# Kernel optimization log

Measured on AMD Instinct MI355X. Metric: run time of the kernel, lower is better.

The kernel has to match this reference:

```python
import jax, jax.numpy as jnp
import numpy as np

# --- model dimensions ---
MAX_UP = 512; MAX_DOWN = 512; MAX_ELEC = MAX_UP + MAX_DOWN  # 1024 orbitals
N_NUC = 128
MAX_CHARGE = 16
TOT_ORB = MAX_CHARGE * (MAX_CHARGE + 1) // 2  # 136
NUM_HEADS = 8; D_HEAD = 32; F = NUM_HEADS * D_HEAD  # 256
L = 4          # num_layers
FN = 256       # nuc_feats dim
SIGMOID_SHIFTS = (2.0, 4.0, 6.0)
E_DIM = 3 + 1 + len(SIGMOID_SHIFTS)  # featurized edge dim = 7


def generate_spd_orbitals(charges):
    """Vectorized form of the scan/fori_loop scatter in the source.
    For nucleus n with charge c: orbitals[cum_charge+i, n, c(c-1)/2+i] = 1 for i<c.
    charges: [N_NUC] int. Returns [MAX_ELEC, N_NUC, TOT_ORB] float32."""
    c = charges.astype(jnp.int32)
    off = jnp.cumsum(c) - c                      # exclusive cumsum (cum_charge)
    prec = c * (c - 1) // 2                      # preceding orbital offset
    i = jnp.arange(MAX_CHARGE, dtype=jnp.int32)
    valid = (i[None, :] < c[:, None])            # [N_NUC, MAX_CHARGE]
    elec = jnp.clip(off[:, None] + i[None, :], 0, MAX_ELEC - 1)
    orbi = jnp.clip(prec[:, None] + i[None, :], 0, TOT_ORB - 1)
    nuc = jnp.broadcast_to(jnp.arange(N_NUC, dtype=jnp.int32)[:, None], (N_NUC, MAX_CHARGE))
    orb = jnp.zeros((MAX_ELEC, N_NUC, TOT_ORB), jnp.float32)
    return orb.at[elec.ravel(), nuc.ravel(), orbi.ravel()].add(valid.ravel().astype(jnp.float32))


def make_permutation(n_up, n_down):
    segments = [0, n_up, MAX_UP, MAX_UP + n_down, MAX_ELEC]
    updates = [0, n_down, -MAX_UP + n_up, 0]
    idx = jnp.arange(MAX_ELEC)
    agg = jnp.zeros_like(idx)
    for lft, r, u in zip(segments[:-1], segments[1:], updates):
        agg = agg + ((idx >= lft) & (idx < r)) * (idx + u)
    return agg


def featurize_real_space_vector(diffs):
    """[N,N,3] -> [N,N,7]: rescaled diffs, log1p(|r|), sigmoid(|r|-shift)."""
    norm = jnp.sqrt(jnp.sum(diffs * diffs, -1, keepdims=True) + 1e-12)
    sig = jnp.concatenate([jax.nn.sigmoid(norm - s) for s in SIGMOID_SHIFTS], -1)
    return jnp.concatenate([diffs / (1.0 + norm), jnp.log1p(norm), sig], -1)


def orb_ln(x):
    """OrbLayerNorm(feat_axis=-1, nuc_axis=1, eps=1.0) on [O, N, F] tensors."""
    mean = jnp.mean(x, -1, keepdims=True)
    var = jnp.var(x, -1, keepdims=True)
    max_var = jnp.max(var, axis=1, keepdims=True)
    return jax.lax.rsqrt(max_var + 1.0) * (x - mean)


def setup_inputs() -> dict:
    key = jax.random.key(0)
    ks = jax.random.split(key, 8)
    coords = jax.random.normal(ks[0], (N_NUC, 3), jnp.float32) * 3.0
    charges = jax.random.randint(ks[1], (N_NUC,), 0, 8)  # sum < MAX_ELEC
    nuc_mask = jnp.ones((N_NUC,), bool)
    nuc_feats = jax.random.normal(ks[2], (N_NUC, FN), jnp.float32)
    orb_mask = jnp.ones((MAX_ELEC,), bool)
    # hk.Linear(num_feats, with_bias=False, TruncatedNormal(stddev=1))
    W_orb = jax.random.truncated_normal(ks[3], -2.0, 2.0, (TOT_ORB, F), jnp.float32)
    W_edge = jax.random.normal(ks[4], (L, E_DIM, NUM_HEADS), jnp.float32) / np.sqrt(E_DIM)
    W_val = jax.random.normal(ks[5], (L, F, F), jnp.float32) / np.sqrt(F)
    W_nuc = jax.random.normal(ks[6], (L, FN, F), jnp.float32) / np.sqrt(FN)
    W_out = jax.random.normal(ks[7], (L, F, F), jnp.float32) / np.sqrt(F)
    return dict(coords=coords, charges=charges, nuc_mask=nuc_mask, n_up=500,
                n_down=480, nuc_feats=nuc_feats, orb_mask=orb_mask, W_orb=W_orb,
                W_edge=W_edge, W_val=W_val, W_nuc=W_nuc, W_out=W_out)


def reference(coords, charges, nuc_mask, n_up, n_down, nuc_feats, orb_mask,
              W_orb, W_edge, W_val, W_nuc, W_out):
    orbital_feats = generate_spd_orbitals(charges)               # [O, N, TOT_ORB]
    perm = make_permutation(int(n_up), int(n_down))
    orbital_feats = orbital_feats[perm]
    feats = jnp.einsum('ont,tf->onf', orbital_feats, W_orb)     # [O, N, F]
    m = (orb_mask[:, None, None] & nuc_mask[None, :, None]).astype(feats.dtype)
    feats = feats * m
    diffs = coords[:, None, :] - coords[None, :, :]              # [N, N, 3]
    nn_mask = nuc_mask[:, None] & nuc_mask[None, :]
    edge = featurize_real_space_vector(diffs) * nn_mask[..., None]  # [N, N, E]
    for l in range(L):
        # --- MaskedMPNNBlock ---
        h = orb_ln(feats)
        vals = jnp.einsum('onf,fg->ong', h, W_val[l]).reshape(MAX_ELEC, N_NUC, NUM_HEADS, D_HEAD)
        ew = jnp.einsum('ije,eh->ijh', edge, W_edge[l]) * nn_mask[..., None]
        msg = jnp.einsum('ijh,ojhd->oihd', ew, vals).reshape(MAX_ELEC, N_NUC, F)
        msg = msg + nuc_feats @ W_nuc[l]
        feats = feats + jnp.einsum('onf,fg->ong', jnp.tanh(orb_ln(msg)), W_out[l])
        feats = feats * m
    return feats
```

## Files before the change

kernel.cpp:

```cpp
#include <hip/hip_runtime.h>
#include <hip/hip_bf16.h>


#define O_TOT 1024

typedef __bf16 bf16x8 __attribute__((ext_vector_type(8)));
typedef float f32x4 __attribute__((ext_vector_type(4)));

static __device__ __forceinline__ unsigned short f2bf(float f) {
  __bf16 b = (__bf16)f;
  unsigned short u;
  __builtin_memcpy(&u, &b, 2);
  return u;
}
static __device__ __forceinline__ float ftanh(float x) {
  float e = __expf(2.f * x);
  return 1.f - 2.f * __builtin_amdgcn_rcpf(e + 1.f);
}

struct alignas(8) US4 { unsigned short a, b, c, d; };

static __device__ __forceinline__ int swzA(int row, int cb) {
  return row * 512 + (cb ^ ((row & 7) << 4) ^ (((row >> 3) & 1) << 5));
}
static __device__ __forceinline__ int swzV(int row, int cb) {
  return row * 256 + (cb ^ ((row & 7) << 4) ^ (((row >> 3) & 1) << 5));
}


__global__ void k_orbmap(const int* __restrict__ charges, const int* __restrict__ n_up_p,
                         const int* __restrict__ n_down_p, int* __restrict__ orb_nuc,
                         int* __restrict__ orb_t) {
  __shared__ int off[129];
  __shared__ int prec[128];
  int tid = threadIdx.x;
  if (tid == 0) {
    int a = 0;
    for (int n = 0; n < 128; ++n) { off[n] = a; a += charges[n]; }
    off[128] = a;
  }
  if (tid < 128) prec[tid] = charges[tid] * (charges[tid] - 1) / 2;
  __syncthreads();
  int nu = *n_up_p, nd = *n_down_p;
  for (int o = tid; o < O_TOT; o += 256) {
    int e;
    if (o < nu) e = o;
    else if (o < 512) e = o + nd;
    else if (o < 512 + nd) e = o + nu - 512;
    else e = o;
    int nn = -1, tt = 0;
    for (int n = 0; n < 128; ++n) {
      if (e >= off[n] && e < off[n + 1]) { nn = n; tt = prec[n] + (e - off[n]); }
    }
    orb_nuc[o] = nn;
    orb_t[o] = tt;
  }
}

__global__ void k_ew(const float* __restrict__ coords, const float* __restrict__ W_edge,
                     unsigned short* __restrict__ ewbf) {
  int i = blockIdx.x, j = threadIdx.x;
  float dx = coords[i * 3 + 0] - coords[j * 3 + 0];
  float dy = coords[i * 3 + 1] - coords[j * 3 + 1];
  float dz = coords[i * 3 + 2] - coords[j * 3 + 2];
  float norm = sqrtf(dx * dx + dy * dy + dz * dz + 1e-12f);
  float inv = 1.f / (1.f + norm);
  float e[7];
  e[0] = dx * inv; e[1] = dy * inv; e[2] = dz * inv;
  e[3] = log1pf(norm);
  e[4] = 1.f / (1.f + expf(-(norm - 2.f)));
  e[5] = 1.f / (1.f + expf(-(norm - 4.f)));
  e[6] = 1.f / (1.f + expf(-(norm - 6.f)));
  const int mt = i >> 4, l16 = i & 15;
  const int k0 = j >> 5, jo = j & 31;
  const int lane = (jo >> 3) * 16 + l16, jj = jo & 7;
  for (int l = 0; l < 4; ++l)
    for (int h = 0; h < 8; ++h) {
      float s = 0.f;
      for (int k = 0; k < 7; ++k) s += e[k] * W_edge[(l * 7 + k) * 8 + h];
      ewbf[(((((l * 8 + h) * 8 + mt) * 4 + k0) * 64) + lane) * 8 + jj] = f2bf(s);
    }
}

__global__ void k_wt(const float* __restrict__ Wv, const float* __restrict__ Wo,
                     unsigned short* __restrict__ WvTf, unsigned short* __restrict__ WoTf) {
  int idx = blockIdx.x * 256 + threadIdx.x;
  const int l = idx >> 16, rem = idx & 65535;
  const int jj = rem & 7, lane = (rem >> 3) & 63, k0 = (rem >> 9) & 7, gt = rem >> 12;
  const int g = gt * 16 + (lane & 15);
  const int f = k0 * 32 + (lane >> 4) * 8 + jj;
  const int src = l * 65536 + f * 256 + g;
  WvTf[idx] = f2bf(Wv[src]);
  WoTf[idx] = f2bf(Wo[src]);
}

__global__ void k_nucbT(const float* __restrict__ nuc_feats, const float* __restrict__ W_nuc,
                        float* __restrict__ nucbT) {
  int b = blockIdx.x;
  int l = b >> 7, i = b & 127;
  int g = threadIdx.x;
  __shared__ float row[256];
  row[g] = nuc_feats[i * 256 + g];
  __syncthreads();
  const float* Wn = W_nuc + l * 65536;
  float s = 0.f;
  for (int f = 0; f < 256; ++f) s += row[f] * Wn[f * 256 + g];
  nucbT[(l * 256 + g) * 128 + i] = s;
}


__global__ __launch_bounds__(512, 2) void k_main(
    float* __restrict__ feats,
    const float* __restrict__ W_orb,
    const unsigned short* __restrict__ WvTf,
    const unsigned short* __restrict__ WoTf,
    const unsigned short* __restrict__ ewbf,
    const float* __restrict__ nucbT,
    const int* __restrict__ orb_nuc, const int* __restrict__ orb_t) {
  __shared__ char SB[65536];
  __shared__ float2 ln2s[8][128];
  __shared__ float red[8];

  const int o = blockIdx.x;
  const int tid = threadIdx.x;
  const int wave = tid >> 6;
  const int lane = tid & 63;
  const int l16 = lane & 15;
  const int kgrp = (lane >> 4) << 3;
  const int rgrp = (lane >> 4) << 2;
  const int w16 = wave * 16;

  const int nn = orb_nuc[o];
  const int tt = orb_t[o];
  float* fo = feats + (size_t)o * 32768;

  f32x4 fr[16];
#pragma unroll
  for (int gt = 0; gt < 16; ++gt) {
    f32x4 v = {0.f, 0.f, 0.f, 0.f};
#pragma unroll
    for (int r = 0; r < 4; ++r)
      if (w16 + rgrp + r == nn) v[r] = W_orb[tt * 256 + gt * 16 + l16];
    fr[gt] = v;
  }

#pragma unroll 1
  for (int l = 0; l < 4; ++l) {
    bf16x8 A[8];
    {
      float s[4] = {0, 0, 0, 0}, q[4] = {0, 0, 0, 0};
#pragma unroll
      for (int gt = 0; gt < 16; ++gt)
#pragma unroll
        for (int r = 0; r < 4; ++r) {
          float v = fr[gt][r];
          s[r] += v; q[r] += v * v;
        }
#pragma unroll
      for (int of = 1; of < 16; of <<= 1)
#pragma unroll
        for (int r = 0; r < 4; ++r) {
          s[r] += __shfl_xor(s[r], of);
          q[r] += __shfl_xor(q[r], of);
        }
      float mean[4], maxv = 0.f;
#pragma unroll
      for (int r = 0; r < 4; ++r) {
        mean[r] = s[r] * (1.f / 256.f);
        const float var = q[r] * (1.f / 256.f) - mean[r] * mean[r];
        maxv = fmaxf(maxv, var);
      }
      maxv = fmaxf(maxv, __shfl_xor(maxv, 16));
      maxv = fmaxf(maxv, __shfl_xor(maxv, 32));
      if (lane == 0) red[wave] = maxv;
#pragma unroll
      for (int gt = 0; gt < 16; ++gt)
#pragma unroll
        for (int r = 0; r < 4; ++r)
          *(unsigned short*)(SB + swzA(w16 + rgrp + r, (gt * 16 + l16) * 2)) =
              f2bf(fr[gt][r] - mean[r]);
#pragma unroll
      for (int k0 = 0; k0 < 8; ++k0)
        A[k0] = *(const bf16x8*)(SB + swzA(w16 + l16, (k0 * 32 + kgrp) * 2));
    }
    __syncthreads();

    {
      float mv = red[0];
#pragma unroll
      for (int w = 1; w < 8; ++w) mv = fmaxf(mv, red[w]);
      const float rstd = rsqrtf(mv + 1.f);
      const unsigned short* Wl = WvTf + (l * 16 * 8 * 64 * 8) + lane * 8;
#pragma unroll
      for (int gt = 0; gt < 16; ++gt) {
        f32x4 acc = {0.f, 0.f, 0.f, 0.f};
        bf16x8 b[4];
#pragma unroll
        for (int k0 = 0; k0 < 4; ++k0)
          b[k0] = *(const bf16x8*)(Wl + (gt * 8 + k0) * 512);
#pragma unroll
        for (int k0 = 0; k0 < 4; ++k0)
          acc = __builtin_amdgcn_mfma_f32_16x16x32_bf16(A[k0], b[k0], acc, 0, 0, 0);
#pragma unroll
        for (int k0 = 0; k0 < 4; ++k0)
          b[k0] = *(const bf16x8*)(Wl + (gt * 8 + k0 + 4) * 512);
#pragma unroll
        for (int k0 = 0; k0 < 4; ++k0)
          acc = __builtin_amdgcn_mfma_f32_16x16x32_bf16(A[k0 + 4], b[k0], acc, 0, 0, 0);
        const int gg = gt * 16 + l16;
        US4 ov{f2bf(acc[0] * rstd), f2bf(acc[1] * rstd), f2bf(acc[2] * rstd),
               f2bf(acc[3] * rstd)};
        *(US4*)(SB + swzV(gg, (w16 + rgrp) * 2)) = ov;
      }
    }
    __syncthreads();

    bf16x8 B0[4], B1[4];
#pragma unroll
    for (int k0 = 0; k0 < 4; ++k0) {
      B0[k0] = *(const bf16x8*)(SB + swzV(wave * 32 + l16, (k0 * 32 + kgrp) * 2));
      B1[k0] = *(const bf16x8*)(SB + swzV(wave * 32 + 16 + l16, (k0 * 32 + kgrp) * 2));
    }
    __syncthreads();

    {
      const unsigned short* ewh = ewbf + ((l * 8 + wave) * 8 * 4 * 64 * 8) + lane * 8;
      const float* nbT = nucbT + l * 32768;
      const int f0 = wave * 32 + l16;
      const int f1 = f0 + 16;
#pragma unroll
      for (int mt = 0; mt < 8; ++mt) {
        const int i0 = mt * 16;
        f32x4 acc0 = {0.f, 0.f, 0.f, 0.f}, acc1 = {0.f, 0.f, 0.f, 0.f};
        {
          bf16x8 a0 = *(const bf16x8*)(ewh + (mt * 4 + 0) * 512);
          bf16x8 a1 = *(const bf16x8*)(ewh + (mt * 4 + 1) * 512);
          acc0 = __builtin_amdgcn_mfma_f32_16x16x32_bf16(a0, B0[0], acc0, 0, 0, 0);
          acc1 = __builtin_amdgcn_mfma_f32_16x16x32_bf16(a0, B1[0], acc1, 0, 0, 0);
          acc0 = __builtin_amdgcn_mfma_f32_16x16x32_bf16(a1, B0[1], acc0, 0, 0, 0);
          acc1 = __builtin_amdgcn_mfma_f32_16x16x32_bf16(a1, B1[1], acc1, 0, 0, 0);
        }
        {
          bf16x8 a0 = *(const bf16x8*)(ewh + (mt * 4 + 2) * 512);
          bf16x8 a1 = *(const bf16x8*)(ewh + (mt * 4 + 3) * 512);
          acc0 = __builtin_amdgcn_mfma_f32_16x16x32_bf16(a0, B0[2], acc0, 0, 0, 0);
          acc1 = __builtin_amdgcn_mfma_f32_16x16x32_bf16(a0, B1[2], acc1, 0, 0, 0);
          acc0 = __builtin_amdgcn_mfma_f32_16x16x32_bf16(a1, B0[3], acc0, 0, 0, 0);
          acc1 = __builtin_amdgcn_mfma_f32_16x16x32_bf16(a1, B1[3], acc1, 0, 0, 0);
        }
        const f32x4 nb0 = *(const f32x4*)(nbT + f0 * 128 + i0 + rgrp);
        const f32x4 nb1 = *(const f32x4*)(nbT + f1 * 128 + i0 + rgrp);
        float sp[4], qp[4];
#pragma unroll
        for (int r = 0; r < 4; ++r) {
          const float v0 = acc0[r] + nb0[r];
          const float v1 = acc1[r] + nb1[r];
          *(unsigned short*)(SB + swzA(i0 + rgrp + r, f0 * 2)) = f2bf(v0);
          *(unsigned short*)(SB + swzA(i0 + rgrp + r, f1 * 2)) = f2bf(v1);
          sp[r] = v0 + v1;
          qp[r] = v0 * v0 + v1 * v1;
        }
#pragma unroll
        for (int of = 1; of < 16; of <<= 1)
#pragma unroll
          for (int r = 0; r < 4; ++r) {
            sp[r] += __shfl_xor(sp[r], of);
            qp[r] += __shfl_xor(qp[r], of);
          }
        if (l16 == 0) {
#pragma unroll
          for (int r = 0; r < 4; ++r)
            ln2s[wave][i0 + rgrp + r] = float2{sp[r], qp[r]};
        }
      }
    }
    __syncthreads();

    {
      float s0 = 0.f, q0 = 0.f, s1v = 0.f, q1v = 0.f;
#pragma unroll
      for (int h = 0; h < 8; ++h) {
        const float2 p0 = ln2s[h][lane];
        const float2 p1 = ln2s[h][lane + 64];
        s0 += p0.x; q0 += p0.y;
        s1v += p1.x; q1v += p1.y;
      }
      const float mean_a = s0 * (1.f / 256.f);
      const float mean_b = s1v * (1.f / 256.f);
      float v0 = q0 * (1.f / 256.f) - mean_a * mean_a;
      float v1 = q1v * (1.f / 256.f) - mean_b * mean_b;
      float mv = fmaxf(v0, v1);
#pragma unroll
      for (int of = 1; of < 64; of <<= 1) mv = fmaxf(mv, __shfl_xor(mv, of));
      const float rstd2 = rsqrtf(mv + 1.f);
      const float meansel = (wave >= 4) ? mean_b : mean_a;
      const float mn = __shfl(meansel, ((wave & 3) << 4) + l16);

      bf16x8 A2[8];
#pragma unroll
      for (int k0 = 0; k0 < 8; ++k0) {
        bf16x8 raw = *(const bf16x8*)(SB + swzA(w16 + l16, (k0 * 32 + kgrp) * 2));
        bf16x8 t;
#pragma unroll
        for (int j = 0; j < 8; ++j)
          t[j] = (__bf16)ftanh(((float)raw[j] - mn) * rstd2);
        A2[k0] = t;
      }

      const unsigned short* Wl = WoTf + (l * 16 * 8 * 64 * 8) + lane * 8;
#pragma unroll
      for (int gt = 0; gt < 16; ++gt) {
        f32x4 acc = fr[gt];
        bf16x8 b[4];
#pragma unroll
        for (int k0 = 0; k0 < 4; ++k0)
          b[k0] = *(const bf16x8*)(Wl + (gt * 8 + k0) * 512);
#pragma unroll
        for (int k0 = 0; k0 < 4; ++k0)
          acc = __builtin_amdgcn_mfma_f32_16x16x32_bf16(A2[k0], b[k0], acc, 0, 0, 0);
#pragma unroll
        for (int k0 = 0; k0 < 4; ++k0)
          b[k0] = *(const bf16x8*)(Wl + (gt * 8 + k0 + 4) * 512);
#pragma unroll
        for (int k0 = 0; k0 < 4; ++k0)
          acc = __builtin_amdgcn_mfma_f32_16x16x32_bf16(A2[k0 + 4], b[k0], acc, 0, 0, 0);
        fr[gt] = acc;
      }
    }
  }

#pragma unroll
  for (int gt = 0; gt < 16; ++gt)
#pragma unroll
    for (int r = 0; r < 4; ++r)
      fo[(w16 + rgrp + r) * 256 + gt * 16 + l16] = fr[gt][r];
}


extern "C" void kernel_launch(void* const* d_in, const int* in_sizes, int n_in,
                              void* d_out, int out_size, void* d_ws, size_t ws_size,
                              hipStream_t stream) {
  const float* coords = (const float*)d_in[0];
  const int* charges = (const int*)d_in[1];
  const int* n_up = (const int*)d_in[3];
  const int* n_down = (const int*)d_in[4];
  const float* nuc_feats = (const float*)d_in[5];
  const float* W_orb = (const float*)d_in[7];
  const float* W_edge = (const float*)d_in[8];
  const float* W_val = (const float*)d_in[9];
  const float* W_nuc = (const float*)d_in[10];
  const float* W_out = (const float*)d_in[11];
  float* out = (float*)d_out;

  char* ws = (char*)d_ws;
  int* orb_nuc = (int*)ws;
  int* orb_t = (int*)(ws + 4096);
  unsigned short* ewbf = (unsigned short*)(ws + 8192);
  unsigned short* WvTf = (unsigned short*)(ws + 8192 + 1048576);
  unsigned short* WoTf = WvTf + 262144;
  float* nucbT = (float*)(ws + 8192 + 1048576 + 1048576);

  k_orbmap<<<dim3(1), dim3(256), 0, stream>>>(charges, n_up, n_down, orb_nuc, orb_t);
  k_ew<<<dim3(128), dim3(128), 0, stream>>>(coords, W_edge, ewbf);
  k_wt<<<dim3(1024), dim3(256), 0, stream>>>(W_val, W_out, WvTf, WoTf);
  k_nucbT<<<dim3(512), dim3(256), 0, stream>>>(nuc_feats, W_nuc, nucbT);
  k_main<<<dim3(O_TOT), dim3(512), 0, stream>>>(out, W_orb, WvTf, WoTf, ewbf, nucbT,
                                                orb_nuc, orb_t);
}
```

Before: 651.2 us.

## Double-buffer weight/edge loads and give V its own LDS buffer to drop a barrier

Result: slower. 790.5 us (+21.4%).

```diff
diff --git a/kernel.cpp b/kernel.cpp
--- a/kernel.cpp
+++ b/kernel.cpp
@@ -118,6 +118,7 @@
     const float* __restrict__ nucbT,
     const int* __restrict__ orb_nuc, const int* __restrict__ orb_t) {
   __shared__ char SB[65536];
+  __shared__ char VBUF[65536];
   __shared__ float2 ln2s[8][128];
   __shared__ float red[8];
 
@@ -186,67 +187,69 @@
     __syncthreads();
 
     {
+      const unsigned short* Wl = WvTf + l * 65536 + lane * 8;
+      bf16x8 bA[8], bB[8];
+#pragma unroll
+      for (int k0 = 0; k0 < 8; ++k0)
+        bA[k0] = *(const bf16x8*)(Wl + k0 * 512);
       float mv = red[0];
 #pragma unroll
       for (int w = 1; w < 8; ++w) mv = fmaxf(mv, red[w]);
       const float rstd = rsqrtf(mv + 1.f);
-      const unsigned short* Wl = WvTf + (l * 16 * 8 * 64 * 8) + lane * 8;
-#pragma unroll
-      for (int gt = 0; gt < 16; ++gt) {
-        f32x4 acc = {0.f, 0.f, 0.f, 0.f};
-        bf16x8 b[4];
-#pragma unroll
-        for (int k0 = 0; k0 < 4; ++k0)
-          b[k0] = *(const bf16x8*)(Wl + (gt * 8 + k0) * 512);
-#pragma unroll
-        for (int k0 = 0; k0 < 4; ++k0)
-          acc = __builtin_amdgcn_mfma_f32_16x16x32_bf16(A[k0], b[k0], acc, 0, 0, 0);
-#pragma unroll
-        for (int k0 = 0; k0 < 4; ++k0)
-          b[k0] = *(const bf16x8*)(Wl + (gt * 8 + k0 + 4) * 512);
-#pragma unroll
-        for (int k0 = 0; k0 < 4; ++k0)
-          acc = __builtin_amdgcn_mfma_f32_16x16x32_bf16(A[k0 + 4], b[k0], acc, 0, 0, 0);
-        const int gg = gt * 16 + l16;
-        US4 ov{f2bf(acc[0] * rstd), f2bf(acc[1] * rstd), f2bf(acc[2] * rstd),
-               f2bf(acc[3] * rstd)};
-        *(US4*)(SB + swzV(gg, (w16 + rgrp) * 2)) = ov;
+#pragma unroll
+      for (int gp = 0; gp < 8; ++gp) {
+#pragma unroll
+        for (int k0 = 0; k0 < 8; ++k0)
+          bB[k0] = *(const bf16x8*)(Wl + ((2 * gp + 1) * 8 + k0) * 512);
+        {
+          f32x4 acc = {0.f, 0.f, 0.f, 0.f};
+#pragma unroll
+          for (int k0 = 0; k0 < 8; ++k0)
+            acc = __builtin_amdgcn_mfma_f32_16x16x32_bf16(A[k0], bA[k0], acc, 0, 0, 0);
+          const int gg = (2 * gp) * 16 + l16;
+          US4 ov{f2bf(acc[0] * rstd), f2bf(acc[1] * rstd), f2bf(acc[2] * rstd),
+                 f2bf(acc[3] * rstd)};
+          *(US4*)(VBUF + swzV(gg, (w16 + rgrp) * 2)) = ov;
+        }
+        if (gp < 7) {
+#pragma unroll
+          for (int k0 = 0; k0 < 8; ++k0)
+            bA[k0] = *(const bf16x8*)(Wl + ((2 * gp + 2) * 8 + k0) * 512);
+        }
+        {
+          f32x4 acc = {0.f, 0.f, 0.f, 0.f};
+#pragma unroll
+          for (int k0 = 0; k0 < 8; ++k0)
+            acc = __builtin_amdgcn_mfma_f32_16x16x32_bf16(A[k0], bB[k0], acc, 0, 0, 0);
+          const int gg = (2 * gp + 1) * 16 + l16;
+          US4 ov{f2bf(acc[0] * rstd), f2bf(acc[1] * rstd), f2bf(acc[2] * rstd),
+                 f2bf(acc[3] * rstd)};
+          *(US4*)(VBUF + swzV(gg, (w16 + rgrp) * 2)) = ov;
+        }
       }
     }
     __syncthreads();
 
-    bf16x8 B0[4], B1[4];
+    bf16x8 VB0[4], VB1[4];
 #pragma unroll
     for (int k0 = 0; k0 < 4; ++k0) {
-      B0[k0] = *(const bf16x8*)(SB + swzV(wave * 32 + l16, (k0 * 32 + kgrp) * 2));
-      B1[k0] = *(const bf16x8*)(SB + swzV(wave * 32 + 16 + l16, (k0 * 32 + kgrp) * 2));
-    }
-    __syncthreads();
+      VB0[k0] = *(const bf16x8*)(VBUF + swzV(wave * 32 + l16, (k0 * 32 + kgrp) * 2));
+      VB1[k0] = *(const bf16x8*)(VBUF + swzV(wave * 32 + 16 + l16, (k0 * 32 + kgrp) * 2));
+    }
 
     {
-      const unsigned short* ewh = ewbf + ((l * 8 + wave) * 8 * 4 * 64 * 8) + lane * 8;
+      const unsigned short* ewh = ewbf + (l * 8 + wave) * 16384 + lane * 8;
       const float* nbT = nucbT + l * 32768;
       const int f0 = wave * 32 + l16;
       const int f1 = f0 + 16;
-#pragma unroll
-      for (int mt = 0; mt < 8; ++mt) {
+
+      auto body = [&](int mt, const bf16x8* a) {
         const int i0 = mt * 16;
         f32x4 acc0 = {0.f, 0.f, 0.f, 0.f}, acc1 = {0.f, 0.f, 0.f, 0.f};
-        {
-          bf16x8 a0 = *(const bf16x8*)(ewh + (mt * 4 + 0) * 512);
-          bf16x8 a1 = *(const bf16x8*)(ewh + (mt * 4 + 1) * 512);
-          acc0 = __builtin_amdgcn_mfma_f32_16x16x32_bf16(a0, B0[0], acc0, 0, 0, 0);
-          acc1 = __builtin_amdgcn_mfma_f32_16x16x32_bf16(a0, B1[0], acc1, 0, 0, 0);
-          acc0 = __builtin_amdgcn_mfma_f32_16x16x32_bf16(a1, B0[1], acc0, 0, 0, 0);
-          acc1 = __builtin_amdgcn_mfma_f32_16x16x32_bf16(a1, B1[1], acc1, 0, 0, 0);
-        }
-        {
-          bf16x8 a0 = *(const bf16x8*)(ewh + (mt * 4 + 2) * 512);
-          bf16x8 a1 = *(const bf16x8*)(ewh + (mt * 4 + 3) * 512);
-          acc0 = __builtin_amdgcn_mfma_f32_16x16x32_bf16(a0, B0[2], acc0, 0, 0, 0);
-          acc1 = __builtin_amdgcn_mfma_f32_16x16x32_bf16(a0, B1[2], acc1, 0, 0, 0);
-          acc0 = __builtin_amdgcn_mfma_f32_16x16x32_bf16(a1, B0[3], acc0, 0, 0, 0);
-          acc1 = __builtin_amdgcn_mfma_f32_16x16x32_bf16(a1, B1[3], acc1, 0, 0, 0);
+#pragma unroll
+        for (int k0 = 0; k0 < 4; ++k0) {
+          acc0 = __builtin_amdgcn_mfma_f32_16x16x32_bf16(a[k0], VB0[k0], acc0, 0, 0, 0);
+          acc1 = __builtin_amdgcn_mfma_f32_16x16x32_bf16(a[k0], VB1[k0], acc1, 0, 0, 0);
         }
         const f32x4 nb0 = *(const f32x4*)(nbT + f0 * 128 + i0 + rgrp);
         const f32x4 nb1 = *(const f32x4*)(nbT + f1 * 128 + i0 + rgrp);
@@ -272,11 +275,35 @@
           for (int r = 0; r < 4; ++r)
             ln2s[wave][i0 + rgrp + r] = float2{sp[r], qp[r]};
         }
+      };
+
+      bf16x8 aA[4], aB[4];
+#pragma unroll
+      for (int k0 = 0; k0 < 4; ++k0)
+        aA[k0] = *(const bf16x8*)(ewh + k0 * 512);
+#pragma unroll
+      for (int mp = 0; mp < 4; ++mp) {
+#pragma unroll
+        for (int k0 = 0; k0 < 4; ++k0)
+          aB[k0] = *(const bf16x8*)(ewh + ((2 * mp + 1) * 4 + k0) * 512);
+        body(2 * mp, aA);
+        if (mp < 3) {
+#pragma unroll
+          for (int k0 = 0; k0 < 4; ++k0)
+            aA[k0] = *(const bf16x8*)(ewh + ((2 * mp + 2) * 4 + k0) * 512);
+        }
+        body(2 * mp + 1, aB);
       }
     }
     __syncthreads();
 
     {
+      const unsigned short* Wl = WoTf + l * 65536 + lane * 8;
+      bf16x8 bA[8], bB[8];
+#pragma unroll
+      for (int k0 = 0; k0 < 8; ++k0)
+        bA[k0] = *(const bf16x8*)(Wl + k0 * 512);
+
       float s0 = 0.f, q0 = 0.f, s1v = 0.f, q1v = 0.f;
 #pragma unroll
       for (int h = 0; h < 8; ++h) {
@@ -307,24 +334,30 @@
         A2[k0] = t;
       }
 
-      const unsigned short* Wl = WoTf + (l * 16 * 8 * 64 * 8) + lane * 8;
-#pragma unroll
-      for (int gt = 0; gt < 16; ++gt) {
-        f32x4 acc = fr[gt];
-        bf16x8 b[4];
-#pragma unroll
-        for (int k0 = 0; k0 < 4; ++k0)
-          b[k0] = *(const bf16x8*)(Wl + (gt * 8 + k0) * 512);
-#pragma unroll
-        for (int k0 = 0; k0 < 4; ++k0)
-          acc = __builtin_amdgcn_mfma_f32_16x16x32_bf16(A2[k0], b[k0], acc, 0, 0, 0);
-#pragma unroll
-        for (int k0 = 0; k0 < 4; ++k0)
-          b[k0] = *(const bf16x8*)(Wl + (gt * 8 + k0 + 4) * 512);
-#pragma unroll
-        for (int k0 = 0; k0 < 4; ++k0)
-          acc = __builtin_amdgcn_mfma_f32_16x16x32_bf16(A2[k0 + 4], b[k0], acc, 0, 0, 0);
-        fr[gt] = acc;
+#pragma unroll
+      for (int gp = 0; gp < 8; ++gp) {
+#pragma unroll
+        for (int k0 = 0; k0 < 8; ++k0)
+          bB[k0] = *(const bf16x8*)(Wl + ((2 * gp + 1) * 8 + k0) * 512);
+        {
+          f32x4 acc = fr[2 * gp];
+#pragma unroll
+          for (int k0 = 0; k0 < 8; ++k0)
+            acc = __builtin_amdgcn_mfma_f32_16x16x32_bf16(A2[k0], bA[k0], acc, 0, 0, 0);
+          fr[2 * gp] = acc;
+        }
+        if (gp < 7) {
+#pragma unroll
+          for (int k0 = 0; k0 < 8; ++k0)
+            bA[k0] = *(const bf16x8*)(Wl + ((2 * gp + 2) * 8 + k0) * 512);
+        }
+        {
+          f32x4 acc = fr[2 * gp + 1];
+#pragma unroll
+          for (int k0 = 0; k0 < 8; ++k0)
+            acc = __builtin_amdgcn_mfma_f32_16x16x32_bf16(A2[k0], bB[k0], acc, 0, 0, 0);
+          fr[2 * gp + 1] = acc;
+        }
       }
     }
   }
```

## Repartition message GEMM so each wave owns nucleus rows across all heads

Applied to the files above, without the earlier changes.

After: 857.7 us. +31.7%, slower.

```diff
diff --git a/kernel.cpp b/kernel.cpp
--- a/kernel.cpp
+++ b/kernel.cpp
@@ -118,8 +118,9 @@
     const float* __restrict__ nucbT,
     const int* __restrict__ orb_nuc, const int* __restrict__ orb_t) {
   __shared__ char SB[65536];
-  __shared__ float2 ln2s[8][128];
-  __shared__ float red[8];
+  __shared__ char VBUF[65536];
+  __shared__ float red1[8];
+  __shared__ float red2[8];
 
   const int o = blockIdx.x;
   const int tid = threadIdx.x;
@@ -172,7 +173,7 @@
       }
       maxv = fmaxf(maxv, __shfl_xor(maxv, 16));
       maxv = fmaxf(maxv, __shfl_xor(maxv, 32));
-      if (lane == 0) red[wave] = maxv;
+      if (lane == 0) red1[wave] = maxv;
 #pragma unroll
       for (int gt = 0; gt < 16; ++gt)
 #pragma unroll
@@ -186,11 +187,11 @@
     __syncthreads();
 
     {
-      float mv = red[0];
-#pragma unroll
-      for (int w = 1; w < 8; ++w) mv = fmaxf(mv, red[w]);
+      float mv = red1[0];
+#pragma unroll
+      for (int w = 1; w < 8; ++w) mv = fmaxf(mv, red1[w]);
       const float rstd = rsqrtf(mv + 1.f);
-      const unsigned short* Wl = WvTf + (l * 16 * 8 * 64 * 8) + lane * 8;
+      const unsigned short* Wl = WvTf + l * 65536 + lane * 8;
 #pragma unroll
       for (int gt = 0; gt < 16; ++gt) {
         f32x4 acc = {0.f, 0.f, 0.f, 0.f};
@@ -210,91 +211,78 @@
         const int gg = gt * 16 + l16;
         US4 ov{f2bf(acc[0] * rstd), f2bf(acc[1] * rstd), f2bf(acc[2] * rstd),
                f2bf(acc[3] * rstd)};
-        *(US4*)(SB + swzV(gg, (w16 + rgrp) * 2)) = ov;
+        *(US4*)(VBUF + swzV(gg, (w16 + rgrp) * 2)) = ov;
       }
     }
     __syncthreads();
 
-    bf16x8 B0[4], B1[4];
-#pragma unroll
-    for (int k0 = 0; k0 < 4; ++k0) {
-      B0[k0] = *(const bf16x8*)(SB + swzV(wave * 32 + l16, (k0 * 32 + kgrp) * 2));
-      B1[k0] = *(const bf16x8*)(SB + swzV(wave * 32 + 16 + l16, (k0 * 32 + kgrp) * 2));
-    }
-    __syncthreads();
-
+    float mean2[4];
     {
-      const unsigned short* ewh = ewbf + ((l * 8 + wave) * 8 * 4 * 64 * 8) + lane * 8;
+      float sacc[4] = {0, 0, 0, 0}, qacc[4] = {0, 0, 0, 0};
       const float* nbT = nucbT + l * 32768;
-      const int f0 = wave * 32 + l16;
-      const int f1 = f0 + 16;
-#pragma unroll
-      for (int mt = 0; mt < 8; ++mt) {
-        const int i0 = mt * 16;
+#pragma unroll
+      for (int h = 0; h < 8; ++h) {
+        const unsigned short* ewh =
+            ewbf + (((l * 8 + h) * 8 + wave) * 4 * 64) * 8 + lane * 8;
+        bf16x8 a[4];
+#pragma unroll
+        for (int k0 = 0; k0 < 4; ++k0)
+          a[k0] = *(const bf16x8*)(ewh + k0 * 512);
+        bf16x8 VB0[4], VB1[4];
+#pragma unroll
+        for (int k0 = 0; k0 < 4; ++k0) {
+          VB0[k0] = *(const bf16x8*)(VBUF + swzV(h * 32 + l16, (k0 * 32 + kgrp) * 2));
+          VB1[k0] = *(const bf16x8*)(VBUF + swzV(h * 32 + 16 + l16, (k0 * 32 + kgrp) * 2));
+        }
         f32x4 acc0 = {0.f, 0.f, 0.f, 0.f}, acc1 = {0.f, 0.f, 0.f, 0.f};
-        {
-          bf16x8 a0 = *(const bf16x8*)(ewh + (mt * 4 + 0) * 512);
-          bf16x8 a1 = *(const bf16x8*)(ewh + (mt * 4 + 1) * 512);
-          acc0 = __builtin_amdgcn_mfma_f32_16x16x32_bf16(a0, B0[0], acc0, 0, 0, 0);
-          acc1 = __builtin_amdgcn_mfma_f32_16x16x32_bf16(a0, B1[0], acc1, 0, 0, 0);
-          acc0 = __builtin_amdgcn_mfma_f32_16x16x32_bf16(a1, B0[1], acc0, 0, 0, 0);
-          acc1 = __builtin_amdgcn_mfma_f32_16x16x32_bf16(a1, B1[1], acc1, 0, 0, 0);
-        }
-        {
-          bf16x8 a0 = *(const bf16x8*)(ewh + (mt * 4 + 2) * 512);
-          bf16x8 a1 = *(const bf16x8*)(ewh + (mt * 4 + 3) * 512);
-          acc0 = __builtin_amdgcn_mfma_f32_16x16x32_bf16(a0, B0[2], acc0, 0, 0, 0);
-          acc1 = __builtin_amdgcn_mfma_f32_16x16x32_bf16(a0, B1[2], acc1, 0, 0, 0);
-          acc0 = __builtin_amdgcn_mfma_f32_16x16x32_bf16(a1, B0[3], acc0, 0, 0, 0);
-          acc1 = __builtin_amdgcn_mfma_f32_16x16x32_bf16(a1, B1[3], acc1, 0, 0, 0);
-        }
-        const f32x4 nb0 = *(const f32x4*)(nbT + f0 * 128 + i0 + rgrp);
-        const f32x4 nb1 = *(const f32x4*)(nbT + f1 * 128 + i0 + rgrp);
-        float sp[4], qp[4];
+#pragma unroll
+        for (int k0 = 0; k0 < 4; ++k0) {
+          acc0 = __builtin_amdgcn_mfma_f32_16x16x32_bf16(a[k0], VB0[k0], acc0, 0, 0, 0);
+          acc1 = __builtin_amdgcn_mfma_f32_16x16x32_bf16(a[k0], VB1[k0], acc1, 0, 0, 0);
+        }
+        const int f0 = h * 32 + l16, f1 = f0 + 16;
+        const f32x4 nb0 = *(const f32x4*)(nbT + f0 * 128 + w16 + rgrp);
+        const f32x4 nb1 = *(const f32x4*)(nbT + f1 * 128 + w16 + rgrp);
 #pragma unroll
         for (int r = 0; r < 4; ++r) {
           const float v0 = acc0[r] + nb0[r];
           const float v1 = acc1[r] + nb1[r];
-          *(unsigned short*)(SB + swzA(i0 + rgrp + r, f0 * 2)) = f2bf(v0);
-          *(unsigned short*)(SB + swzA(i0 + rgrp + r, f1 * 2)) = f2bf(v1);
-          sp[r] = v0 + v1;
-          qp[r] = v0 * v0 + v1 * v1;
-        }
-#pragma unroll
-        for (int of = 1; of < 16; of <<= 1)
-#pragma unroll
-          for (int r = 0; r < 4; ++r) {
-            sp[r] += __shfl_xor(sp[r], of);
-            qp[r] += __shfl_xor(qp[r], of);
-          }
-        if (l16 == 0) {
-#pragma unroll
-          for (int r = 0; r < 4; ++r)
-            ln2s[wave][i0 + rgrp + r] = float2{sp[r], qp[r]};
-        }
-      }
+          *(unsigned short*)(SB + swzA(w16 + rgrp + r, f0 * 2)) = f2bf(v0);
+          *(unsigned short*)(SB + swzA(w16 + rgrp + r, f1 * 2)) = f2bf(v1);
+          sacc[r] += v0 + v1;
+          qacc[r] += v0 * v0 + v1 * v1;
+        }
+      }
+#pragma unroll
+      for (int of = 1; of < 16; of <<= 1)
+#pragma unroll
+        for (int r = 0; r < 4; ++r) {
+          sacc[r] += __shfl_xor(sacc[r], of);
+          qacc[r] += __shfl_xor(qacc[r], of);
+        }
+      float maxv = 0.f;
+#pragma unroll
+      for (int r = 0; r < 4; ++r) {
+        mean2[r] = sacc[r] * (1.f / 256.f);
+        maxv = fmaxf(maxv, qacc[r] * (1.f / 256.f) - mean2[r] * mean2[r]);
+      }
+      maxv = fmaxf(maxv, __shfl_xor(maxv, 16));
+      maxv = fmaxf(maxv, __shfl_xor(maxv, 32));
+      if (lane == 0) red2[wave] = maxv;
     }
     __syncthreads();
 
     {
-      float s0 = 0.f, q0 = 0.f, s1v = 0.f, q1v = 0.f;
-#pragma unroll
-      for (int h = 0; h < 8; ++h) {
-        const float2 p0 = ln2s[h][lane];
-        const float2 p1 = ln2s[h][lane + 64];
-        s0 += p0.x; q0 += p0.y;
-        s1v += p1.x; q1v += p1.y;
-      }
-      const float mean_a = s0 * (1.f / 256.f);
-      const float mean_b = s1v * (1.f / 256.f);
-      float v0 = q0 * (1.f / 256.f) - mean_a * mean_a;
-      float v1 = q1v * (1.f / 256.f) - mean_b * mean_b;
-      float mv = fmaxf(v0, v1);
-#pragma unroll
-      for (int of = 1; of < 64; of <<= 1) mv = fmaxf(mv, __shfl_xor(mv, of));
+      float mv = red2[0];
+#pragma unroll
+      for (int w = 1; w < 8; ++w) mv = fmaxf(mv, red2[w]);
       const float rstd2 = rsqrtf(mv + 1.f);
-      const float meansel = (wave >= 4) ? mean_b : mean_a;
-      const float mn = __shfl(meansel, ((wave & 3) << 4) + l16);
+      const int rsel = l16 & 3;
+      const float mcand = (rsel == 0)   ? mean2[0]
+                          : (rsel == 1) ? mean2[1]
+                          : (rsel == 2) ? mean2[2]
+                                        : mean2[3];
+      const float mn = __shfl(mcand, ((l16 >> 2) << 4) + l16);
 
       bf16x8 A2[8];
 #pragma unroll
@@ -307,7 +295,7 @@
         A2[k0] = t;
       }
 
-      const unsigned short* Wl = WoTf + (l * 16 * 8 * 64 * 8) + lane * 8;
+      const unsigned short* Wl = WoTf + l * 65536 + lane * 8;
 #pragma unroll
       for (int gt = 0; gt < 16; ++gt) {
         f32x4 acc = fr[gt];
```

## Stage Wv and Wo weight halves into LDS via global_load_lds

Applied to the files above, without the earlier changes.

Result: faster. 568.1 us (-12.8%).

```diff
diff --git a/kernel.cpp b/kernel.cpp
--- a/kernel.cpp
+++ b/kernel.cpp
@@ -118,6 +118,7 @@
     const float* __restrict__ nucbT,
     const int* __restrict__ orb_nuc, const int* __restrict__ orb_t) {
   __shared__ char SB[65536];
+  __shared__ char WS[65536];
   __shared__ float2 ln2s[8][128];
   __shared__ float red[8];
 
@@ -134,6 +135,16 @@
   const int tt = orb_t[o];
   float* fo = feats + (size_t)o * 32768;
 
+  auto stage64 = [&](const unsigned short* gsrc) {
+#pragma unroll
+    for (int s = 0; s < 8; ++s)
+      __builtin_amdgcn_global_load_lds(
+          (const __attribute__((address_space(1))) void*)(gsrc + s * 4096 +
+                                                          wave * 512 + lane * 8),
+          (__attribute__((address_space(3))) void*)(WS + s * 8192 + wave * 1024),
+          16, 0, 0);
+  };
+
   f32x4 fr[16];
 #pragma unroll
   for (int gt = 0; gt < 16; ++gt) {
@@ -146,6 +157,8 @@
 
 #pragma unroll 1
   for (int l = 0; l < 4; ++l) {
+    stage64(WvTf + l * 65536);
+
     bf16x8 A[8];
     {
       float s[4] = {0, 0, 0, 0}, q[4] = {0, 0, 0, 0};
@@ -185,33 +198,59 @@
     }
     __syncthreads();
 
+    float rstd;
     {
       float mv = red[0];
 #pragma unroll
       for (int w = 1; w < 8; ++w) mv = fmaxf(mv, red[w]);
-      const float rstd = rsqrtf(mv + 1.f);
-      const unsigned short* Wl = WvTf + (l * 16 * 8 * 64 * 8) + lane * 8;
-#pragma unroll
-      for (int gt = 0; gt < 16; ++gt) {
-        f32x4 acc = {0.f, 0.f, 0.f, 0.f};
-        bf16x8 b[4];
-#pragma unroll
-        for (int k0 = 0; k0 < 4; ++k0)
-          b[k0] = *(const bf16x8*)(Wl + (gt * 8 + k0) * 512);
-#pragma unroll
-        for (int k0 = 0; k0 < 4; ++k0)
-          acc = __builtin_amdgcn_mfma_f32_16x16x32_bf16(A[k0], b[k0], acc, 0, 0, 0);
-#pragma unroll
-        for (int k0 = 0; k0 < 4; ++k0)
-          b[k0] = *(const bf16x8*)(Wl + (gt * 8 + k0 + 4) * 512);
-#pragma unroll
-        for (int k0 = 0; k0 < 4; ++k0)
-          acc = __builtin_amdgcn_mfma_f32_16x16x32_bf16(A[k0 + 4], b[k0], acc, 0, 0, 0);
-        const int gg = gt * 16 + l16;
-        US4 ov{f2bf(acc[0] * rstd), f2bf(acc[1] * rstd), f2bf(acc[2] * rstd),
-               f2bf(acc[3] * rstd)};
-        *(US4*)(SB + swzV(gg, (w16 + rgrp) * 2)) = ov;
-      }
+      rstd = rsqrtf(mv + 1.f);
+    }
+
+#pragma unroll
+    for (int gt = 0; gt < 8; ++gt) {
+      f32x4 acc = {0.f, 0.f, 0.f, 0.f};
+      bf16x8 b[4];
+#pragma unroll
+      for (int k0 = 0; k0 < 4; ++k0)
+        b[k0] = *(const bf16x8*)(WS + ((gt * 8 + k0) << 10) + lane * 16);
+#pragma unroll
+      for (int k0 = 0; k0 < 4; ++k0)
+        acc = __builtin_amdgcn_mfma_f32_16x16x32_bf16(A[k0], b[k0], acc, 0, 0, 0);
+#pragma unroll
+      for (int k0 = 0; k0 < 4; ++k0)
+        b[k0] = *(const bf16x8*)(WS + ((gt * 8 + k0 + 4) << 10) + lane * 16);
+#pragma unroll
+      for (int k0 = 0; k0 < 4; ++k0)
+        acc = __builtin_amdgcn_mfma_f32_16x16x32_bf16(A[k0 + 4], b[k0], acc, 0, 0, 0);
+      const int gg = gt * 16 + l16;
+      US4 ov{f2bf(acc[0] * rstd), f2bf(acc[1] * rstd), f2bf(acc[2] * rstd),
+             f2bf(acc[3] * rstd)};
+      *(US4*)(SB + swzV(gg, (w16 + rgrp) * 2)) = ov;
+    }
+    __syncthreads();
+    stage64(WvTf + l * 65536 + 32768);
+    __syncthreads();
+
+#pragma unroll
+    for (int gt = 8; gt < 16; ++gt) {
+      f32x4 acc = {0.f, 0.f, 0.f, 0.f};
+      bf16x8 b[4];
+#pragma unroll
+      for (int k0 = 0; k0 < 4; ++k0)
+        b[k0] = *(const bf16x8*)(WS + (((gt - 8) * 8 + k0) << 10) + lane * 16);
+#pragma unroll
+      for (int k0 = 0; k0 < 4; ++k0)
+        acc = __builtin_amdgcn_mfma_f32_16x16x32_bf16(A[k0], b[k0], acc, 0, 0, 0);
+#pragma unroll
+      for (int k0 = 0; k0 < 4; ++k0)
+        b[k0] = *(const bf16x8*)(WS + (((gt - 8) * 8 + k0 + 4) << 10) + lane * 16);
+#pragma unroll
+      for (int k0 = 0; k0 < 4; ++k0)
+        acc = __builtin_amdgcn_mfma_f32_16x16x32_bf16(A[k0 + 4], b[k0], acc, 0, 0, 0);
+      const int gg = gt * 16 + l16;
+      US4 ov{f2bf(acc[0] * rstd), f2bf(acc[1] * rstd), f2bf(acc[2] * rstd),
+             f2bf(acc[3] * rstd)};
+      *(US4*)(SB + swzV(gg, (w16 + rgrp) * 2)) = ov;
     }
     __syncthreads();
 
@@ -222,6 +261,8 @@
       B1[k0] = *(const bf16x8*)(SB + swzV(wave * 32 + 16 + l16, (k0 * 32 + kgrp) * 2));
     }
     __syncthreads();
+
+    stage64(WoTf + l * 65536);
 
     {
       const unsigned short* ewh = ewbf + ((l * 8 + wave) * 8 * 4 * 64 * 8) + lane * 8;
@@ -276,6 +317,7 @@
     }
     __syncthreads();
 
+    bf16x8 A2[8];
     {
       float s0 = 0.f, q0 = 0.f, s1v = 0.f, q1v = 0.f;
 #pragma unroll
@@ -295,8 +337,6 @@
       const float rstd2 = rsqrtf(mv + 1.f);
       const float meansel = (wave >= 4) ? mean_b : mean_a;
       const float mn = __shfl(meansel, ((wave & 3) << 4) + l16);
-
-      bf16x8 A2[8];
 #pragma unroll
       for (int k0 = 0; k0 < 8; ++k0) {
         bf16x8 raw = *(const bf16x8*)(SB + swzA(w16 + l16, (k0 * 32 + kgrp) * 2));
@@ -306,27 +346,48 @@
           t[j] = (__bf16)ftanh(((float)raw[j] - mn) * rstd2);
         A2[k0] = t;
       }
-
-      const unsigned short* Wl = WoTf + (l * 16 * 8 * 64 * 8) + lane * 8;
-#pragma unroll
-      for (int gt = 0; gt < 16; ++gt) {
-        f32x4 acc = fr[gt];
-        bf16x8 b[4];
-#pragma unroll
-        for (int k0 = 0; k0 < 4; ++k0)
-          b[k0] = *(const bf16x8*)(Wl + (gt * 8 + k0) * 512);
-#pragma unroll
-        for (int k0 = 0; k0 < 4; ++k0)
-          acc = __builtin_amdgcn_mfma_f32_16x16x32_bf16(A2[k0], b[k0], acc, 0, 0, 0);
-#pragma unroll
-        for (int k0 = 0; k0 < 4; ++k0)
-          b[k0] = *(const bf16x8*)(Wl + (gt * 8 + k0 + 4) * 512);
-#pragma unroll
-        for (int k0 = 0; k0 < 4; ++k0)
-          acc = __builtin_amdgcn_mfma_f32_16x16x32_bf16(A2[k0 + 4], b[k0], acc, 0, 0, 0);
-        fr[gt] = acc;
-      }
-    }
+    }
+#pragma unroll
+    for (int gt = 0; gt < 8; ++gt) {
+      f32x4 acc = fr[gt];
+      bf16x8 b[4];
+#pragma unroll
+      for (int k0 = 0; k0 < 4; ++k0)
+        b[k0] = *(const bf16x8*)(WS + ((gt * 8 + k0) << 10) + lane * 16);
+#pragma unroll
+      for (int k0 = 0; k0 < 4; ++k0)
+        acc = __builtin_amdgcn_mfma_f32_16x16x32_bf16(A2[k0], b[k0], acc, 0, 0, 0);
+#pragma unroll
+      for (int k0 = 0; k0 < 4; ++k0)
+        b[k0] = *(const bf16x8*)(WS + ((gt * 8 + k0 + 4) << 10) + lane * 16);
+#pragma unroll
+      for (int k0 = 0; k0 < 4; ++k0)
+        acc = __builtin_amdgcn_mfma_f32_16x16x32_bf16(A2[k0 + 4], b[k0], acc, 0, 0, 0);
+      fr[gt] = acc;
+    }
+    __syncthreads();
+    stage64(WoTf + l * 65536 + 32768);
+    __syncthreads();
+
+#pragma unroll
+    for (int gt = 8; gt < 16; ++gt) {
+      f32x4 acc = fr[gt];
+      bf16x8 b[4];
+#pragma unroll
+      for (int k0 = 0; k0 < 4; ++k0)
+        b[k0] = *(const bf16x8*)(WS + (((gt - 8) * 8 + k0) << 10) + lane * 16);
+#pragma unroll
+      for (int k0 = 0; k0 < 4; ++k0)
+        acc = __builtin_amdgcn_mfma_f32_16x16x32_bf16(A2[k0], b[k0], acc, 0, 0, 0);
+#pragma unroll
+      for (int k0 = 0; k0 < 4; ++k0)
+        b[k0] = *(const bf16x8*)(WS + (((gt - 8) * 8 + k0 + 4) << 10) + lane * 16);
+#pragma unroll
+      for (int k0 = 0; k0 < 4; ++k0)
+        acc = __builtin_amdgcn_mfma_f32_16x16x32_bf16(A2[k0 + 4], b[k0], acc, 0, 0, 0);
+      fr[gt] = acc;
+    }
+    __syncthreads();
   }
 
 #pragma unroll
```
